# Performance work log

Hardware: AMD Instinct MI355X
Metric: run time of the kernel (lower is better)

The kernel has to match this reference:

```python
import jax, jax.numpy as jnp
import numpy as np

B, T, C, H = 2, 2048, 1024, 16
HD = C // H  # head dim = 64


def setup_inputs() -> dict:
    key = jax.random.key(0)
    k1, k2, k3 = jax.random.split(key, 3)
    x = jax.random.normal(k1, (B, T, C), dtype=jnp.float32)
    W_attn = jax.random.normal(k2, (C, 3 * C), dtype=jnp.float32) * (C ** -0.5)
    W_proj = jax.random.normal(k3, (C, C), dtype=jnp.float32) * (C ** -0.5)
    b_proj = jnp.zeros((C,), dtype=jnp.float32)
    return {"x": x, "W_attn": W_attn, "W_proj": W_proj, "b_proj": b_proj}


def reference(x, W_attn, W_proj, b_proj):
    Bv, Tv, Cv = x.shape
    qkv = x @ W_attn  # [B, T, 3C]  (no bias: config.bias=False)
    # NOTE: source splits as k, q, v (k first!)
    k, q, v = jnp.split(qkv, 3, axis=2)
    # [B, H, T, HD]
    q = q.reshape(Bv, Tv, H, HD).transpose(0, 2, 1, 3)
    k = k.reshape(Bv, Tv, H, HD).transpose(0, 2, 1, 3)
    v = v.reshape(Bv, Tv, H, HD).transpose(0, 2, 1, 3)
    wei = jnp.einsum('bhqd,bhkd->bhqk', q, k) * (HD ** -0.5)
    causal = jnp.tril(jnp.ones((Tv, Tv), dtype=bool))
    wei = jnp.where(causal, wei, -jnp.inf)
    wei = jax.nn.softmax(wei, axis=-1)
    # dropout = 0.0 (eval) -> identity
    out = jnp.einsum('bhqk,bhkd->bhqd', wei, v)
    out = out.transpose(0, 2, 1, 3).reshape(Bv, Tv, Cv)
    out = out @ W_proj + b_proj
    return out
```

## Files before the change

kernel.cpp:

```cpp
#include <hip/hip_runtime.h>

typedef __attribute__((ext_vector_type(8))) short short8;
typedef __attribute__((ext_vector_type(4))) short short4v;
typedef __attribute__((ext_vector_type(4))) float float4v;

#define T_SEQ 2048
#define CDIM 1024
#define NHEAD 16
#define HDIM 64
#define LROW 40

__device__ __forceinline__ unsigned short f2bf(float f) {
    unsigned u = __builtin_bit_cast(unsigned, f);
    u += 0x7FFF + ((u >> 16) & 1);
    return (unsigned short)(u >> 16);
}

__global__ __launch_bounds__(256) void convert_f32_bf16_vec(
    const float* __restrict__ in, unsigned short* __restrict__ out) {
    int i = blockIdx.x * 256 + threadIdx.x;
    float4 v = ((const float4*)in)[i];
    ushort4 o;
    o.x = f2bf(v.x); o.y = f2bf(v.y); o.z = f2bf(v.z); o.w = f2bf(v.w);
    ((ushort4*)out)[i] = o;
}

__global__ __launch_bounds__(256) void transpose_f32_bf16(
    const float* __restrict__ in, unsigned short* __restrict__ out, int K, int N) {
    __shared__ float tile[32][33];
    int kb = blockIdx.x * 32, nb = blockIdx.y * 32;
    int tx = threadIdx.x & 31, ty = threadIdx.x >> 5;
    for (int r = 0; r < 4; r++)
        tile[ty + r * 8][tx] = in[(size_t)(kb + ty + r * 8) * N + nb + tx];
    __syncthreads();
    for (int r = 0; r < 4; r++)
        out[(size_t)(nb + ty + r * 8) * K + kb + tx] = f2bf(tile[tx][ty + r * 8]);
}

__global__ __launch_bounds__(256) void gemm_qkv(
    const unsigned short* __restrict__ A, const unsigned short* __restrict__ Bt,
    unsigned short* __restrict__ dK, unsigned short* __restrict__ dQ,
    unsigned short* __restrict__ dV) {
    const int K = 1024;
    const int NITER = K / 32;
    __shared__ unsigned short sA[2][128 * LROW];
    __shared__ unsigned short sB[2][128 * LROW];
    int tid = threadIdx.x, wave = tid >> 6, lane = tid & 63;
    int quad = lane >> 4, l16 = lane & 15;
    int wm = wave >> 1, wn = wave & 1;
    int blockM = blockIdx.y * 128, blockN = blockIdx.x * 128;
    int rlane = lane >> 2, seg = lane & 3;
    bool swapAB = (blockN >= 2048);

    const unsigned short* gA = A + (size_t)blockM * K;
    const unsigned short* gB = Bt + (size_t)blockN * K;

    float4v acc[4][4] = {};
    uint4 ra[2], rb[2];

    int srow[2], soff[2];
    for (int i = 0; i < 2; i++) {
        srow[i] = wave * 32 + i * 16 + rlane;
        soff[i] = srow[i] * LROW + seg * 8;
    }

    for (int i = 0; i < 2; i++) {
        ra[i] = *(const uint4*)(gA + (size_t)srow[i] * K + seg * 8);
        rb[i] = *(const uint4*)(gB + (size_t)srow[i] * K + seg * 8);
    }
    for (int i = 0; i < 2; i++) {
        *(uint4*)(sA[0] + soff[i]) = ra[i];
        *(uint4*)(sB[0] + soff[i]) = rb[i];
    }

    for (int it = 0; it < NITER; it++) {
        int cur = it & 1;
        __syncthreads();
        if (it + 1 < NITER) {
            int kb = (it + 1) * 32;
            for (int i = 0; i < 2; i++) {
                ra[i] = *(const uint4*)(gA + (size_t)srow[i] * K + kb + seg * 8);
                rb[i] = *(const uint4*)(gB + (size_t)srow[i] * K + kb + seg * 8);
            }
        }
        const unsigned short* cA = sA[cur];
        const unsigned short* cB = sB[cur];
        short8 af[4], bf[4];
        for (int i = 0; i < 4; i++)
            af[i] = *(const short8*)(cA + (wm * 64 + i * 16 + l16) * LROW + quad * 8);
        for (int j = 0; j < 4; j++)
            bf[j] = *(const short8*)(cB + (wn * 64 + j * 16 + l16) * LROW + quad * 8);
        if (!swapAB) {
            for (int i = 0; i < 4; i++)
                for (int j = 0; j < 4; j++)
                    acc[i][j] = __builtin_amdgcn_mfma_f32_16x16x32_bf16(
                        af[i], bf[j], acc[i][j], 0, 0, 0);
        } else {
            for (int i = 0; i < 4; i++)
                for (int j = 0; j < 4; j++)
                    acc[i][j] = __builtin_amdgcn_mfma_f32_16x16x32_bf16(
                        bf[j], af[i], acc[i][j], 0, 0, 0);
        }
        if (it + 1 < NITER) {
            int nxt = cur ^ 1;
            for (int i = 0; i < 2; i++) {
                *(uint4*)(sA[nxt] + soff[i]) = ra[i];
                *(uint4*)(sB[nxt] + soff[i]) = rb[i];
            }
        }
    }

    if (!swapAB) {
        const float QSCL = 0.18033688011112042f;
        for (int i = 0; i < 4; i++)
            for (int j = 0; j < 4; j++)
                for (int r = 0; r < 4; r++) {
                    int m = blockM + wm * 64 + i * 16 + quad * 4 + r;
                    int n = blockN + wn * 64 + j * 16 + l16;
                    int part = n >> 10, c = n & 1023;
                    int h = c >> 6, d = c & 63;
                    int bb = m >> 11, t = m & 2047;
                    int bh = bb * NHEAD + h;
                    if (part == 0) {
                        dK[(((size_t)bh * T_SEQ + t) << 6) + d] = f2bf(acc[i][j][r]);
                    } else {
                        dQ[(((size_t)bh * T_SEQ + t) << 6) + d] =
                            f2bf(acc[i][j][r] * QSCL);
                    }
                }
    } else {
        for (int i = 0; i < 4; i++)
            for (int j = 0; j < 4; j++)
                for (int r = 0; r < 4; r++) {
                    int n = blockN + wn * 64 + j * 16 + quad * 4 + r;
                    int m = blockM + wm * 64 + i * 16 + l16;
                    int c = n & 1023;
                    int h = c >> 6, d = c & 63;
                    int bb = m >> 11, t = m & 2047;
                    int bh = bb * NHEAD + h;
                    dV[((size_t)bh * HDIM + d) * T_SEQ + t] = f2bf(acc[i][j][r]);
                }
    }
}

__global__ __launch_bounds__(256) void gemm_proj64(
    const unsigned short* __restrict__ A, const unsigned short* __restrict__ Bt,
    const float* __restrict__ bias, float* __restrict__ out) {
    const int K = 1024;
    const int NITER = K / 32;
    __shared__ unsigned short sA[2][64 * LROW];
    __shared__ unsigned short sB[2][64 * LROW];
    int tid = threadIdx.x, wave = tid >> 6, lane = tid & 63;
    int quad = lane >> 4, l16 = lane & 15;
    int wm = wave >> 1, wn = wave & 1;
    int blockM = blockIdx.y * 64, blockN = blockIdx.x * 64;
    int rlane = lane >> 2, seg = lane & 3;

    const unsigned short* gA = A + (size_t)blockM * K;
    const unsigned short* gB = Bt + (size_t)blockN * K;

    float4v acc[2][2] = {};
    uint4 r2[2];
    const unsigned short* gsrc[2];
    unsigned short* ldst[2][2];
    for (int i = 0; i < 2; i++) {
        int c = wave * 2 + i;
        int isB = c >> 2, cc = c & 3;
        int row = cc * 16 + rlane;
        gsrc[i] = (isB ? gB : gA) + (size_t)row * K + seg * 8;
        for (int b = 0; b < 2; b++)
            ldst[i][b] = (isB ? sB[b] : sA[b]) + row * LROW + seg * 8;
    }

    for (int i = 0; i < 2; i++) r2[i] = *(const uint4*)gsrc[i];
    for (int i = 0; i < 2; i++) *(uint4*)ldst[i][0] = r2[i];

    for (int it = 0; it < NITER; it++) {
        int cur = it & 1;
        __syncthreads();
        if (it + 1 < NITER) {
            int kb = (it + 1) * 32;
            for (int i = 0; i < 2; i++) r2[i] = *(const uint4*)(gsrc[i] + kb);
        }
        const unsigned short* cA = sA[cur];
        const unsigned short* cB = sB[cur];
        short8 af[2], bf[2];
        for (int i = 0; i < 2; i++)
            af[i] = *(const short8*)(cA + (wm * 32 + i * 16 + l16) * LROW + quad * 8);
        for (int j = 0; j < 2; j++)
            bf[j] = *(const short8*)(cB + (wn * 32 + j * 16 + l16) * LROW + quad * 8);
        for (int i = 0; i < 2; i++)
            for (int j = 0; j < 2; j++)
                acc[i][j] = __builtin_amdgcn_mfma_f32_16x16x32_bf16(
                    af[i], bf[j], acc[i][j], 0, 0, 0);
        if (it + 1 < NITER) {
            int nxt = cur ^ 1;
            for (int i = 0; i < 2; i++) *(uint4*)ldst[i][nxt] = r2[i];
        }
    }

    for (int i = 0; i < 2; i++)
        for (int j = 0; j < 2; j++)
            for (int r = 0; r < 4; r++) {
                int m = blockM + wm * 32 + i * 16 + quad * 4 + r;
                int n = blockN + wn * 32 + j * 16 + l16;
                out[(size_t)m * CDIM + n] = acc[i][j][r] + bias[n];
            }
}

__global__ __launch_bounds__(256) void attn_fwd(
    const unsigned short* __restrict__ Qp, const unsigned short* __restrict__ Kp,
    const unsigned short* __restrict__ Vt, unsigned short* __restrict__ att) {
    __shared__ unsigned short sK[2][64 * 72];
    __shared__ unsigned short sV[2][64 * 72];
    int tid = threadIdx.x, wave = tid >> 6, lane = tid & 63;
    int quad = lane >> 4, l16 = lane & 15;
    int bh = blockIdx.x;
    int bb = bh >> 4, h = bh & 15;
    size_t baseQ = (size_t)bh * T_SEQ * HDIM;
    size_t baseV = (size_t)bh * HDIM * T_SEQ;
    const int NT = T_SEQ / 64;
    int row4 = tid >> 2, seg = tid & 3;

    for (int pass = 0; pass < 2; pass++) {
        int xt = (pass == 0) ? blockIdx.y : (NT - 1 - blockIdx.y);
        int qb = xt * 64;
        int qrow = qb + wave * 16 + l16;

        const unsigned short* qr = Qp + baseQ + (size_t)qrow * HDIM;
        short8 qf0 = *(const short8*)(qr + quad * 8);
        short8 qf1 = *(const short8*)(qr + 32 + quad * 8);

        float4v o[4] = {};
        float lsum = 0.f;
        int nt = xt + 1;

        uint4 ka, kb2, va, vb;
        {
            const unsigned short* gk = Kp + baseQ + (size_t)row4 * HDIM + seg * 16;
            const unsigned short* gv = Vt + baseV + (size_t)row4 * T_SEQ + seg * 16;
            ka = *(const uint4*)gk; kb2 = *(const uint4*)(gk + 8);
            va = *(const uint4*)gv; vb = *(const uint4*)(gv + 8);
        }
        __syncthreads();
        *(uint4*)(sK[0] + row4 * 72 + seg * 16) = ka;
        *(uint4*)(sK[0] + row4 * 72 + seg * 16 + 8) = kb2;
        *(uint4*)(sV[0] + row4 * 72 + seg * 16) = va;
        *(uint4*)(sV[0] + row4 * 72 + seg * 16 + 8) = vb;

        for (int t = 0; t < nt; t++) {
            int cur = t & 1;
            __syncthreads();
            if (t + 1 < nt) {
                const unsigned short* gk =
                    Kp + baseQ + (size_t)((t + 1) * 64 + row4) * HDIM + seg * 16;
                const unsigned short* gv =
                    Vt + baseV + (size_t)row4 * T_SEQ + (t + 1) * 64 + seg * 16;
                ka = *(const uint4*)gk; kb2 = *(const uint4*)(gk + 8);
                va = *(const uint4*)gv; vb = *(const uint4*)(gv + 8);
            }

            const unsigned short* cK = sK[cur];
            const unsigned short* cV = sV[cur];
            float4v s[4];
            for (int sub = 0; sub < 4; sub++) {
                short8 kf0 = *(const short8*)(cK + (sub * 16 + l16) * 72 + quad * 8);
                short8 kf1 =
                    *(const short8*)(cK + (sub * 16 + l16) * 72 + 32 + quad * 8);
                float4v z = {};
                z = __builtin_amdgcn_mfma_f32_16x16x32_bf16(kf0, qf0, z, 0, 0, 0);
                z = __builtin_amdgcn_mfma_f32_16x16x32_bf16(kf1, qf1, z, 0, 0, 0);
                s[sub] = z;
            }

            bool need_mask = (t * 64 + 63) > (qb + wave * 16);
            float p[16];
            for (int sub = 0; sub < 4; sub++)
                for (int r = 0; r < 4; r++) {
                    float v = s[sub][r];
                    if (need_mask) {
                        int kg = t * 64 + sub * 16 + quad * 4 + r;
                        v = (kg <= qrow) ? v : -1e30f;
                    }
                    p[sub * 4 + r] = v;
                }
            unsigned ub[16];
            for (int i = 0; i < 16; i++) {
                float e = exp2f(p[i] - 16.0f);
                unsigned u = __builtin_bit_cast(unsigned, e) & 0xffff0000u;
                ub[i] = u;
                lsum += __builtin_bit_cast(float, u);
            }

            for (int sub = 0; sub < 4; sub++) {
                unsigned lo = __builtin_amdgcn_perm(ub[sub * 4 + 1], ub[sub * 4 + 0],
                                                    0x07060302u);
                unsigned hi = __builtin_amdgcn_perm(ub[sub * 4 + 3], ub[sub * 4 + 2],
                                                    0x07060302u);
                uint2 packed = {lo, hi};
                short4v pf = __builtin_bit_cast(short4v, packed);
                for (int dc = 0; dc < 4; dc++) {
                    short4v vf = *(const short4v*)(
                        cV + (dc * 16 + l16) * 72 + sub * 16 + quad * 4);
                    o[dc] = __builtin_amdgcn_mfma_f32_16x16x16bf16_1k(
                        vf, pf, o[dc], 0, 0, 0);
                }
            }

            if (t + 1 < nt) {
                int nxt = cur ^ 1;
                *(uint4*)(sK[nxt] + row4 * 72 + seg * 16) = ka;
                *(uint4*)(sK[nxt] + row4 * 72 + seg * 16 + 8) = kb2;
                *(uint4*)(sV[nxt] + row4 * 72 + seg * 16) = va;
                *(uint4*)(sV[nxt] + row4 * 72 + seg * 16 + 8) = vb;
            }
        }

        lsum += __shfl_xor(lsum, 16);
        lsum += __shfl_xor(lsum, 32);
        float inv = 1.0f / lsum;

        __syncthreads();
        for (int dc = 0; dc < 4; dc++) {
            short4v ov;
            for (int r = 0; r < 4; r++) ov[r] = (short)f2bf(o[dc][r] * inv);
            *(short4v*)(sK[0] + wave * 1152 + l16 * 72 + dc * 16 + quad * 4) = ov;
        }
        __syncthreads();
        int orow = lane >> 2, oseg = lane & 3;
        uint4 a = *(const uint4*)(sK[0] + wave * 1152 + orow * 72 + oseg * 16);
        uint4 b = *(const uint4*)(sK[0] + wave * 1152 + orow * 72 + oseg * 16 + 8);
        unsigned short* dst = att +
            (size_t)(bb * T_SEQ + qb + wave * 16 + orow) * CDIM + h * HDIM +
            oseg * 16;
        *(uint4*)dst = a;
        *(uint4*)(dst + 8) = b;
    }
}

extern "C" void kernel_launch(void* const* d_in, const int* in_sizes, int n_in,
                              void* d_out, int out_size, void* d_ws, size_t ws_size,
                              hipStream_t stream) {
    const float* x      = (const float*)d_in[0];
    const float* W_attn = (const float*)d_in[1];
    const float* W_proj = (const float*)d_in[2];
    const float* b_proj = (const float*)d_in[3];
    float* out = (float*)d_out;

    unsigned short* xb   = (unsigned short*)d_ws;
    unsigned short* WaT  = xb  + 4096 * 1024;
    unsigned short* WpT  = WaT + 3072 * 1024;
    unsigned short* Karr = WpT + 1024 * 1024;
    unsigned short* Qarr = Karr + 2 * 16 * 2048 * 64;
    unsigned short* Varr = Qarr + 2 * 16 * 2048 * 64;
    unsigned short* attb = Varr + 2 * 16 * 2048 * 64;

    convert_f32_bf16_vec<<<4096, 256, 0, stream>>>(x, xb);
    transpose_f32_bf16<<<dim3(32, 96), 256, 0, stream>>>(W_attn, WaT, 1024, 3072);
    transpose_f32_bf16<<<dim3(32, 32), 256, 0, stream>>>(W_proj, WpT, 1024, 1024);
    gemm_qkv<<<dim3(24, 32), 256, 0, stream>>>(xb, WaT, Karr, Qarr, Varr);
    attn_fwd<<<dim3(32, 16), 256, 0, stream>>>(Qarr, Karr, Varr, attb);
    gemm_proj64<<<dim3(16, 64), 256, 0, stream>>>(attb, WpT, b_proj, out);
}
```

Baseline: 203.5 us.

## Process 128 query rows per attention block to reuse K/V tiles

The attention kernel no longer runs two passes of 64 query rows per block. Each block now handles one 128-row query tile, with each wave owning two 16-row subtiles, so every K/V tile loaded into LDS and every K fragment read from it serves twice as many query rows. Load balance across the causal triangle comes from ordering the 128-row tiles from longest to shortest, and a wave skips key tiles lying entirely above its diagonal. The epilogue writes all 128 rows at once through LDS. Both GEMMs also switch to precomputed, incrementing global pointers and LDS offsets to cut address arithmetic. The cost is more accumulator registers per wave, which may lower occupancy, and coarser per-block work units.

```diff
diff --git a/kernel.cpp b/kernel.cpp
--- a/kernel.cpp
+++ b/kernel.cpp
@@ -58,38 +58,38 @@
     float4v acc[4][4] = {};
     uint4 ra[2], rb[2];
 
-    int srow[2], soff[2];
-    for (int i = 0; i < 2; i++) {
-        srow[i] = wave * 32 + i * 16 + rlane;
-        soff[i] = srow[i] * LROW + seg * 8;
-    }
-
-    for (int i = 0; i < 2; i++) {
-        ra[i] = *(const uint4*)(gA + (size_t)srow[i] * K + seg * 8);
-        rb[i] = *(const uint4*)(gB + (size_t)srow[i] * K + seg * 8);
-    }
-    for (int i = 0; i < 2; i++) {
-        *(uint4*)(sA[0] + soff[i]) = ra[i];
-        *(uint4*)(sB[0] + soff[i]) = rb[i];
-    }
+    int srow0 = wave * 32 + rlane, srow1 = srow0 + 16;
+    int soff0 = srow0 * LROW + seg * 8, soff1 = srow1 * LROW + seg * 8;
+    const unsigned short* pA0 = gA + (size_t)srow0 * K + seg * 8;
+    const unsigned short* pA1 = gA + (size_t)srow1 * K + seg * 8;
+    const unsigned short* pB0 = gB + (size_t)srow0 * K + seg * 8;
+    const unsigned short* pB1 = gB + (size_t)srow1 * K + seg * 8;
+
+    ra[0] = *(const uint4*)pA0; ra[1] = *(const uint4*)pA1;
+    rb[0] = *(const uint4*)pB0; rb[1] = *(const uint4*)pB1;
+    *(uint4*)(sA[0] + soff0) = ra[0];
+    *(uint4*)(sA[0] + soff1) = ra[1];
+    *(uint4*)(sB[0] + soff0) = rb[0];
+    *(uint4*)(sB[0] + soff1) = rb[1];
+
+    int aoff = (wm * 64 + l16) * LROW + quad * 8;
+    int boff = (wn * 64 + l16) * LROW + quad * 8;
 
     for (int it = 0; it < NITER; it++) {
         int cur = it & 1;
         __syncthreads();
         if (it + 1 < NITER) {
-            int kb = (it + 1) * 32;
-            for (int i = 0; i < 2; i++) {
-                ra[i] = *(const uint4*)(gA + (size_t)srow[i] * K + kb + seg * 8);
-                rb[i] = *(const uint4*)(gB + (size_t)srow[i] * K + kb + seg * 8);
-            }
+            pA0 += 32; pA1 += 32; pB0 += 32; pB1 += 32;
+            ra[0] = *(const uint4*)pA0; ra[1] = *(const uint4*)pA1;
+            rb[0] = *(const uint4*)pB0; rb[1] = *(const uint4*)pB1;
         }
         const unsigned short* cA = sA[cur];
         const unsigned short* cB = sB[cur];
         short8 af[4], bf[4];
         for (int i = 0; i < 4; i++)
-            af[i] = *(const short8*)(cA + (wm * 64 + i * 16 + l16) * LROW + quad * 8);
+            af[i] = *(const short8*)(cA + aoff + i * 16 * LROW);
         for (int j = 0; j < 4; j++)
-            bf[j] = *(const short8*)(cB + (wn * 64 + j * 16 + l16) * LROW + quad * 8);
+            bf[j] = *(const short8*)(cB + boff + j * 16 * LROW);
         if (!swapAB) {
             for (int i = 0; i < 4; i++)
                 for (int j = 0; j < 4; j++)
@@ -103,10 +103,10 @@
         }
         if (it + 1 < NITER) {
             int nxt = cur ^ 1;
-            for (int i = 0; i < 2; i++) {
-                *(uint4*)(sA[nxt] + soff[i]) = ra[i];
-                *(uint4*)(sB[nxt] + soff[i]) = rb[i];
-            }
+            *(uint4*)(sA[nxt] + soff0) = ra[0];
+            *(uint4*)(sA[nxt] + soff1) = ra[1];
+            *(uint4*)(sB[nxt] + soff0) = rb[0];
+            *(uint4*)(sB[nxt] + soff1) = rb[1];
         }
     }
 
@@ -161,41 +161,45 @@
 
     float4v acc[2][2] = {};
     uint4 r2[2];
-    const unsigned short* gsrc[2];
-    unsigned short* ldst[2][2];
-    for (int i = 0; i < 2; i++) {
-        int c = wave * 2 + i;
-        int isB = c >> 2, cc = c & 3;
-        int row = cc * 16 + rlane;
-        gsrc[i] = (isB ? gB : gA) + (size_t)row * K + seg * 8;
-        for (int b = 0; b < 2; b++)
-            ldst[i][b] = (isB ? sB[b] : sA[b]) + row * LROW + seg * 8;
-    }
-
-    for (int i = 0; i < 2; i++) r2[i] = *(const uint4*)gsrc[i];
-    for (int i = 0; i < 2; i++) *(uint4*)ldst[i][0] = r2[i];
+
+    int c0 = wave * 2, c1 = wave * 2 + 1;
+    int isB0 = c0 >> 2, cc0 = c0 & 3, row0 = cc0 * 16 + rlane;
+    int isB1 = c1 >> 2, cc1 = c1 & 3, row1 = cc1 * 16 + rlane;
+    const unsigned short* p0 = (isB0 ? gB : gA) + (size_t)row0 * K + seg * 8;
+    const unsigned short* p1 = (isB1 ? gB : gA) + (size_t)row1 * K + seg * 8;
+    int so0 = row0 * LROW + seg * 8, so1 = row1 * LROW + seg * 8;
+
+    r2[0] = *(const uint4*)p0;
+    r2[1] = *(const uint4*)p1;
+    *(uint4*)((isB0 ? sB[0] : sA[0]) + so0) = r2[0];
+    *(uint4*)((isB1 ? sB[0] : sA[0]) + so1) = r2[1];
+
+    int aoff = (wm * 32 + l16) * LROW + quad * 8;
+    int boff = (wn * 32 + l16) * LROW + quad * 8;
 
     for (int it = 0; it < NITER; it++) {
         int cur = it & 1;
         __syncthreads();
         if (it + 1 < NITER) {
-            int kb = (it + 1) * 32;
-            for (int i = 0; i < 2; i++) r2[i] = *(const uint4*)(gsrc[i] + kb);
+            p0 += 32; p1 += 32;
+            r2[0] = *(const uint4*)p0;
+            r2[1] = *(const uint4*)p1;
         }
         const unsigned short* cA = sA[cur];
         const unsigned short* cB = sB[cur];
         short8 af[2], bf[2];
         for (int i = 0; i < 2; i++)
-            af[i] = *(const short8*)(cA + (wm * 32 + i * 16 + l16) * LROW + quad * 8);
+            af[i] = *(const short8*)(cA + aoff + i * 16 * LROW);
         for (int j = 0; j < 2; j++)
-            bf[j] = *(const short8*)(cB + (wn * 32 + j * 16 + l16) * LROW + quad * 8);
+            bf[j] = *(const short8*)(cB + boff + j * 16 * LROW);
         for (int i = 0; i < 2; i++)
             for (int j = 0; j < 2; j++)
                 acc[i][j] = __builtin_amdgcn_mfma_f32_16x16x32_bf16(
                     af[i], bf[j], acc[i][j], 0, 0, 0);
         if (it + 1 < NITER) {
             int nxt = cur ^ 1;
-            for (int i = 0; i < 2; i++) *(uint4*)ldst[i][nxt] = r2[i];
+            *(uint4*)((isB0 ? sB[nxt] : sA[nxt]) + so0) = r2[0];
+            *(uint4*)((isB1 ? sB[nxt] : sA[nxt]) + so1) = r2[1];
         }
     }
 
@@ -219,123 +223,147 @@
     int bb = bh >> 4, h = bh & 15;
     size_t baseQ = (size_t)bh * T_SEQ * HDIM;
     size_t baseV = (size_t)bh * HDIM * T_SEQ;
-    const int NT = T_SEQ / 64;
     int row4 = tid >> 2, seg = tid & 3;
 
-    for (int pass = 0; pass < 2; pass++) {
-        int xt = (pass == 0) ? blockIdx.y : (NT - 1 - blockIdx.y);
-        int qb = xt * 64;
-        int qrow = qb + wave * 16 + l16;
-
-        const unsigned short* qr = Qp + baseQ + (size_t)qrow * HDIM;
-        short8 qf0 = *(const short8*)(qr + quad * 8);
-        short8 qf1 = *(const short8*)(qr + 32 + quad * 8);
-
-        float4v o[4] = {};
-        float lsum = 0.f;
-        int nt = xt + 1;
-
-        uint4 ka, kb2, va, vb;
-        {
-            const unsigned short* gk = Kp + baseQ + (size_t)row4 * HDIM + seg * 16;
-            const unsigned short* gv = Vt + baseV + (size_t)row4 * T_SEQ + seg * 16;
+    int y = blockIdx.y;
+    int xt = (y < 8) ? (15 - y) : (y - 8);
+    int qb = xt * 128;
+    int nt = 2 * xt + 2;
+
+    int q0 = qb + wave * 32 + l16;
+    const unsigned short* qr0 = Qp + baseQ + (size_t)q0 * HDIM;
+    short8 qf[2][2];
+    qf[0][0] = *(const short8*)(qr0 + quad * 8);
+    qf[0][1] = *(const short8*)(qr0 + 32 + quad * 8);
+    qf[1][0] = *(const short8*)(qr0 + 16 * HDIM + quad * 8);
+    qf[1][1] = *(const short8*)(qr0 + 16 * HDIM + 32 + quad * 8);
+
+    float4v o[2][4] = {};
+    float lsum[2] = {0.f, 0.f};
+
+    uint4 ka, kb2, va, vb;
+    {
+        const unsigned short* gk = Kp + baseQ + (size_t)row4 * HDIM + seg * 16;
+        const unsigned short* gv = Vt + baseV + (size_t)row4 * T_SEQ + seg * 16;
+        ka = *(const uint4*)gk; kb2 = *(const uint4*)(gk + 8);
+        va = *(const uint4*)gv; vb = *(const uint4*)(gv + 8);
+    }
+    *(uint4*)(sK[0] + row4 * 72 + seg * 16) = ka;
+    *(uint4*)(sK[0] + row4 * 72 + seg * 16 + 8) = kb2;
+    *(uint4*)(sV[0] + row4 * 72 + seg * 16) = va;
+    *(uint4*)(sV[0] + row4 * 72 + seg * 16 + 8) = vb;
+
+    for (int t = 0; t < nt; t++) {
+        int cur = t & 1;
+        __syncthreads();
+        if (t + 1 < nt) {
+            const unsigned short* gk =
+                Kp + baseQ + (size_t)((t + 1) * 64 + row4) * HDIM + seg * 16;
+            const unsigned short* gv =
+                Vt + baseV + (size_t)row4 * T_SEQ + (t + 1) * 64 + seg * 16;
             ka = *(const uint4*)gk; kb2 = *(const uint4*)(gk + 8);
             va = *(const uint4*)gv; vb = *(const uint4*)(gv + 8);
         }
-        __syncthreads();
-        *(uint4*)(sK[0] + row4 * 72 + seg * 16) = ka;
-        *(uint4*)(sK[0] + row4 * 72 + seg * 16 + 8) = kb2;
-        *(uint4*)(sV[0] + row4 * 72 + seg * 16) = va;
-        *(uint4*)(sV[0] + row4 * 72 + seg * 16 + 8) = vb;
-
-        for (int t = 0; t < nt; t++) {
-            int cur = t & 1;
-            __syncthreads();
-            if (t + 1 < nt) {
-                const unsigned short* gk =
-                    Kp + baseQ + (size_t)((t + 1) * 64 + row4) * HDIM + seg * 16;
-                const unsigned short* gv =
-                    Vt + baseV + (size_t)row4 * T_SEQ + (t + 1) * 64 + seg * 16;
-                ka = *(const uint4*)gk; kb2 = *(const uint4*)(gk + 8);
-                va = *(const uint4*)gv; vb = *(const uint4*)(gv + 8);
-            }
-
+        if (t * 64 <= qb + wave * 32 + 31) {
             const unsigned short* cK = sK[cur];
             const unsigned short* cV = sV[cur];
-            float4v s[4];
+
+            short8 kf[4][2];
             for (int sub = 0; sub < 4; sub++) {
-                short8 kf0 = *(const short8*)(cK + (sub * 16 + l16) * 72 + quad * 8);
-                short8 kf1 =
+                kf[sub][0] = *(const short8*)(cK + (sub * 16 + l16) * 72 + quad * 8);
+                kf[sub][1] =
                     *(const short8*)(cK + (sub * 16 + l16) * 72 + 32 + quad * 8);
-                float4v z = {};
-                z = __builtin_amdgcn_mfma_f32_16x16x32_bf16(kf0, qf0, z, 0, 0, 0);
-                z = __builtin_amdgcn_mfma_f32_16x16x32_bf16(kf1, qf1, z, 0, 0, 0);
-                s[sub] = z;
             }
-
-            bool need_mask = (t * 64 + 63) > (qb + wave * 16);
-            float p[16];
-            for (int sub = 0; sub < 4; sub++)
-                for (int r = 0; r < 4; r++) {
-                    float v = s[sub][r];
-                    if (need_mask) {
-                        int kg = t * 64 + sub * 16 + quad * 4 + r;
-                        v = (kg <= qrow) ? v : -1e30f;
+            float4v sc[2][4];
+            for (int s2 = 0; s2 < 2; s2++)
+                for (int sub = 0; sub < 4; sub++) {
+                    float4v z = {};
+                    z = __builtin_amdgcn_mfma_f32_16x16x32_bf16(
+                        kf[sub][0], qf[s2][0], z, 0, 0, 0);
+                    z = __builtin_amdgcn_mfma_f32_16x16x32_bf16(
+                        kf[sub][1], qf[s2][1], z, 0, 0, 0);
+                    sc[s2][sub] = z;
+                }
+
+            unsigned ub[2][16];
+            for (int s2 = 0; s2 < 2; s2++) {
+                int qrow = qb + wave * 32 + s2 * 16 + l16;
+                bool need_mask = (t * 64 + 63) > (qb + wave * 32 + s2 * 16);
+                for (int sub = 0; sub < 4; sub++)
+                    for (int r = 0; r < 4; r++) {
+                        float v = sc[s2][sub][r];
+                        if (need_mask) {
+                            int kg = t * 64 + sub * 16 + quad * 4 + r;
+                            v = (kg <= qrow) ? v : -1e30f;
+                        }
+                        float e = exp2f(v - 16.0f);
+                        unsigned u = __builtin_bit_cast(unsigned, e) & 0xffff0000u;
+                        ub[s2][sub * 4 + r] = u;
+                        lsum[s2] += __builtin_bit_cast(float, u);
                     }
-                    p[sub * 4 + r] = v;
-                }
-            unsigned ub[16];
-            for (int i = 0; i < 16; i++) {
-                float e = exp2f(p[i] - 16.0f);
-                unsigned u = __builtin_bit_cast(unsigned, e) & 0xffff0000u;
-                ub[i] = u;
-                lsum += __builtin_bit_cast(float, u);
             }
 
             for (int sub = 0; sub < 4; sub++) {
-                unsigned lo = __builtin_amdgcn_perm(ub[sub * 4 + 1], ub[sub * 4 + 0],
-                                                    0x07060302u);
-                unsigned hi = __builtin_amdgcn_perm(ub[sub * 4 + 3], ub[sub * 4 + 2],
-                                                    0x07060302u);
-                uint2 packed = {lo, hi};
-                short4v pf = __builtin_bit_cast(short4v, packed);
+                unsigned lo0 = __builtin_amdgcn_perm(ub[0][sub * 4 + 1],
+                                                     ub[0][sub * 4 + 0], 0x07060302u);
+                unsigned hi0 = __builtin_amdgcn_perm(ub[0][sub * 4 + 3],
+                                                     ub[0][sub * 4 + 2], 0x07060302u);
+                unsigned lo1 = __builtin_amdgcn_perm(ub[1][sub * 4 + 1],
+                                                     ub[1][sub * 4 + 0], 0x07060302u);
+                unsigned hi1 = __builtin_amdgcn_perm(ub[1][sub * 4 + 3],
+                                                     ub[1][sub * 4 + 2], 0x07060302u);
+                uint2 pk0 = {lo0, hi0}, pk1 = {lo1, hi1};
+                short4v pf0 = __builtin_bit_cast(short4v, pk0);
+                short4v pf1 = __builtin_bit_cast(short4v, pk1);
                 for (int dc = 0; dc < 4; dc++) {
                     short4v vf = *(const short4v*)(
                         cV + (dc * 16 + l16) * 72 + sub * 16 + quad * 4);
-                    o[dc] = __builtin_amdgcn_mfma_f32_16x16x16bf16_1k(
-                        vf, pf, o[dc], 0, 0, 0);
+                    o[0][dc] = __builtin_amdgcn_mfma_f32_16x16x16bf16_1k(
+                        vf, pf0, o[0][dc], 0, 0, 0);
+                    o[1][dc] = __builtin_amdgcn_mfma_f32_16x16x16bf16_1k(
+                        vf, pf1, o[1][dc], 0, 0, 0);
                 }
             }
-
-            if (t + 1 < nt) {
-                int nxt = cur ^ 1;
-                *(uint4*)(sK[nxt] + row4 * 72 + seg * 16) = ka;
-                *(uint4*)(sK[nxt] + row4 * 72 + seg * 16 + 8) = kb2;
-                *(uint4*)(sV[nxt] + row4 * 72 + seg * 16) = va;
-                *(uint4*)(sV[nxt] + row4 * 72 + seg * 16 + 8) = vb;
-            }
-        }
-
-        lsum += __shfl_xor(lsum, 16);
-        lsum += __shfl_xor(lsum, 32);
-        float inv = 1.0f / lsum;
-
-        __syncthreads();
+        }
+        if (t + 1 < nt) {
+            int nxt = cur ^ 1;
+            *(uint4*)(sK[nxt] + row4 * 72 + seg * 16) = ka;
+            *(uint4*)(sK[nxt] + row4 * 72 + seg * 16 + 8) = kb2;
+            *(uint4*)(sV[nxt] + row4 * 72 + seg * 16) = va;
+            *(uint4*)(sV[nxt] + row4 * 72 + seg * 16 + 8) = vb;
+        }
+    }
+
+    for (int s2 = 0; s2 < 2; s2++) {
+        lsum[s2] += __shfl_xor(lsum[s2], 16);
+        lsum[s2] += __shfl_xor(lsum[s2], 32);
+    }
+    float inv0 = 1.0f / lsum[0], inv1 = 1.0f / lsum[1];
+
+    __syncthreads();
+    unsigned short* ep = &sK[0][0];
+    for (int s2 = 0; s2 < 2; s2++) {
+        float inv = s2 ? inv1 : inv0;
         for (int dc = 0; dc < 4; dc++) {
             short4v ov;
-            for (int r = 0; r < 4; r++) ov[r] = (short)f2bf(o[dc][r] * inv);
-            *(short4v*)(sK[0] + wave * 1152 + l16 * 72 + dc * 16 + quad * 4) = ov;
-        }
-        __syncthreads();
-        int orow = lane >> 2, oseg = lane & 3;
-        uint4 a = *(const uint4*)(sK[0] + wave * 1152 + orow * 72 + oseg * 16);
-        uint4 b = *(const uint4*)(sK[0] + wave * 1152 + orow * 72 + oseg * 16 + 8);
-        unsigned short* dst = att +
-            (size_t)(bb * T_SEQ + qb + wave * 16 + orow) * CDIM + h * HDIM +
-            oseg * 16;
-        *(uint4*)dst = a;
-        *(uint4*)(dst + 8) = b;
-    }
+            for (int r = 0; r < 4; r++) ov[r] = (short)f2bf(o[s2][dc][r] * inv);
+            *(short4v*)(ep + (wave * 32 + s2 * 16 + l16) * 72 + dc * 16 + quad * 4) =
+                ov;
+        }
+    }
+    __syncthreads();
+    int orow = tid >> 1, half = tid & 1;
+    const unsigned short* src = ep + orow * 72 + half * 32;
+    uint4 a0 = *(const uint4*)(src);
+    uint4 a1 = *(const uint4*)(src + 8);
+    uint4 a2 = *(const uint4*)(src + 16);
+    uint4 a3 = *(const uint4*)(src + 24);
+    unsigned short* dst =
+        att + (size_t)(bb * T_SEQ + qb + orow) * CDIM + h * HDIM + half * 32;
+    *(uint4*)dst = a0;
+    *(uint4*)(dst + 8) = a1;
+    *(uint4*)(dst + 16) = a2;
+    *(uint4*)(dst + 24) = a3;
 }
 
 extern "C" void kernel_launch(void* const* d_in, const int* in_sizes, int n_in,
```

After: 225.1 us. 10.6% more time.
